# Optimization experiments

Measured on AMD Instinct MI355X. Metric: run time of the kernel, lower is better.

## Reference

```python
import jax, jax.numpy as jnp
import numpy as np

EPS = 1e-5

def _ln(x, g, b):
    mu = jnp.mean(x, axis=-1, keepdims=True)
    var = jnp.mean(jnp.square(x - mu), axis=-1, keepdims=True)
    return (x - mu) * jax.lax.rsqrt(var + EPS) * g + b

def setup_inputs() -> dict:
    B, T, D, E, H, M = 2, 2048, 1024, 8, 512, 2048
    key = jax.random.key(0)
    ks = jax.random.split(key, 24)
    s = 0.02
    inp = {}
    inp['x'] = jax.random.normal(ks[0], (B, T, D), jnp.float32)
    flat = jnp.arange(M, dtype=jnp.int32) * 2  # unique token ids over B*T
    inp['index_b'] = flat // T
    inp['index_t'] = flat % T
    # shared SwiGLU (hidden = H)
    inp['sw1'] = jax.random.normal(ks[1], (H, D), jnp.float32) * s
    inp['sb1'] = jnp.zeros((H,), jnp.float32)
    inp['sw2'] = jax.random.normal(ks[2], (H, D), jnp.float32) * s
    inp['sb2'] = jnp.zeros((H,), jnp.float32)
    inp['sw3'] = jax.random.normal(ks[3], (D, H), jnp.float32) * s
    inp['sb3'] = jnp.zeros((D,), jnp.float32)
    inp['s_ln_g'] = jnp.ones((H,), jnp.float32)
    inp['s_ln_b'] = jnp.zeros((H,), jnp.float32)
    # gates
    inp['sg_w'] = jax.random.normal(ks[4], (1, D), jnp.float32) * s
    inp['sg_b'] = jnp.zeros((1,), jnp.float32)
    inp['eg_w'] = jax.random.normal(ks[5], (E, D), jnp.float32) * s
    inp['eg_b'] = jnp.zeros((E,), jnp.float32)
    inp['exp_bias'] = jnp.zeros((E,), jnp.float32)
    # per-expert SwiGLU stacks
    inp['ew1'] = jax.random.normal(ks[6], (E, H, D), jnp.float32) * s
    inp['eb1'] = jnp.zeros((E, H), jnp.float32)
    inp['ew2'] = jax.random.normal(ks[7], (E, H, D), jnp.float32) * s
    inp['eb2'] = jnp.zeros((E, H), jnp.float32)
    inp['ew3'] = jax.random.normal(ks[8], (E, D, H), jnp.float32) * s
    inp['eb3'] = jnp.zeros((E, D), jnp.float32)
    inp['sel_ln_g'] = jnp.ones((H,), jnp.float32)
    inp['sel_ln_b'] = jnp.zeros((H,), jnp.float32)
    return inp

def _forward(x, index_b, index_t, sw1, sb1, sw2, sb2, sw3, sb3, s_ln_g, s_ln_b,
             sg_w, sg_b, eg_w, eg_b, exp_bias, ew1, eb1, ew2, eb2, ew3, eb3,
             sel_ln_g, sel_ln_b):
    # shared SwiGLU over all tokens: [B,T,D]
    x1 = jnp.einsum('btd,hd->bth', x, sw1) + sb1
    x2 = jnp.einsum('btd,hd->bth', x, sw2) + sb2
    sh = _ln(jax.nn.silu(x1) * x2, s_ln_g, s_ln_b)
    shared_out = jnp.einsum('bth,dh->btd', sh, sw3) + sb3
    # MoE tokens
    x_moe = x[index_b, index_t]  # [M,D]
    shared_scores = jax.nn.sigmoid(x_moe @ sg_w.T + sg_b)       # [M,1]
    expert_scores = jax.nn.sigmoid(x_moe @ eg_w.T + eg_b)       # [M,E]
    top1_idx = jnp.argmax(expert_scores + exp_bias, axis=-1)    # [M]
    top1_score = jnp.take_along_axis(expert_scores, top1_idx[:, None], axis=-1)  # [M,1]
    weights = jax.nn.softmax(jnp.concatenate([shared_scores, top1_score], axis=-1), axis=-1)
    shared_w, expert_w = weights[:, 0], weights[:, 1]
    shared_moe_out = shared_out[index_b, index_t] * shared_w[:, None]
    # per-expert SwiGLU computed densely for all E, then token selects its expert
    h1 = jnp.einsum('md,ehd->meh', x_moe, ew1) + eb1  # [M,E,H]
    h2 = jnp.einsum('md,ehd->meh', x_moe, ew2) + eb2
    z = _ln(jax.nn.silu(h1) * h2, sel_ln_g, sel_ln_b)
    out_all = jnp.einsum('meh,edh->med', z, ew3) + eb3  # [M,E,D]
    expert_out = jnp.take_along_axis(out_all, top1_idx[:, None, None], axis=1)[:, 0]  # [M,D]
    expert_moe_out = expert_out * expert_w[:, None]
    final_out = shared_out.at[index_b, index_t].set(shared_moe_out + expert_moe_out)
    return final_out

def reference(x, index_b, index_t, sw1, sb1, sw2, sb2, sw3, sb3, s_ln_g, s_ln_b,
              sg_w, sg_b, eg_w, eg_b, exp_bias, ew1, eb1, ew2, eb2, ew3, eb3,
              sel_ln_g, sel_ln_b):
    return _forward(x, index_b, index_t, sw1, sb1, sw2, sb2, sw3, sb3, s_ln_g, s_ln_b,
                    sg_w, sg_b, eg_w, eg_b, exp_bias, ew1, eb1, ew2, eb2, ew3, eb3,
                    sel_ln_g, sel_ln_b)
```

## Files before the change

kernel.cpp:

```cpp
#include <hip/hip_runtime.h>
#include <cstdint>

typedef unsigned short u16;
typedef __bf16 bf16x8 __attribute__((ext_vector_type(8)));
typedef float f32x4 __attribute__((ext_vector_type(4)));

#define T_SEQ  2048
#define D_DIM  1024
#define H_DIM  512
#define E_NUM  8
#define M_TOK  2048
#define BT_TOK 4096
#define MAXP   3072

static __device__ __forceinline__ u16 f2bf(float f) {
    union { float f; uint32_t u; } v; v.f = f;
    uint32_t u = v.u;
    return (u16)((u + 0x7FFFu + ((u >> 16) & 1u)) >> 16);
}
static __device__ __forceinline__ uint32_t pack2r(float a, float b) {
    union { float f; uint32_t u; } x, y; x.f = a; y.f = b;
    return ((x.u + 0x8000u) >> 16) | ((y.u + 0x8000u) & 0xffff0000u);
}

__global__ __launch_bounds__(256)
void gating_kernel(const float* __restrict__ x,
                   const int* __restrict__ ib, const int* __restrict__ itx,
                   const float* __restrict__ sgw, const float* __restrict__ sgb,
                   const float* __restrict__ egw, const float* __restrict__ egb,
                   const float* __restrict__ ebias,
                   float* __restrict__ shw, float* __restrict__ expw,
                   int* __restrict__ top1, int* __restrict__ rowidx)
{
    int m = blockIdx.x, tid = threadIdx.x;
    __shared__ float xs[D_DIM];
    __shared__ float sc[9];
    int row = ib[m] * T_SEQ + itx[m];
    if (tid == 0) rowidx[m] = row;
    const float* xr = x + (size_t)row * D_DIM;
    ((float4*)xs)[tid] = ((const float4*)xr)[tid];
    __syncthreads();
    int lane = tid & 63, w = tid >> 6;
    for (int sidx = w; sidx < 9; sidx += 4) {
        const float* wr = (sidx == 0) ? sgw : (egw + (size_t)(sidx - 1) * D_DIM);
        float acc = 0.f;
        for (int i = lane; i < D_DIM; i += 64) acc += xs[i] * wr[i];
        #pragma unroll
        for (int o = 32; o > 0; o >>= 1) acc += __shfl_xor(acc, o);
        if (lane == 0) sc[sidx] = acc;
    }
    __syncthreads();
    if (tid == 0) {
        float ss = 1.f / (1.f + expf(-(sc[0] + sgb[0])));
        float es[E_NUM];
        float best = -1e30f; int bi = 0;
        #pragma unroll
        for (int e = 0; e < E_NUM; ++e) {
            es[e] = 1.f / (1.f + expf(-(sc[1 + e] + egb[e])));
            float t = es[e] + ebias[e];
            if (t > best) { best = t; bi = e; }
        }
        float ts = es[bi];
        shw[m]  = 1.f / (1.f + expf(ts - ss));
        expw[m] = 1.f / (1.f + expf(ss - ts));
        top1[m] = bi;
    }
}

__global__ void bucket_kernel(const int* __restrict__ top1,
                              int* __restrict__ base, int* __restrict__ cnt,
                              int* __restrict__ perm)
{
    __shared__ int lc[E_NUM], lb[E_NUM + 1], cur[E_NUM];
    int tid = threadIdx.x;
    if (tid < E_NUM) { lc[tid] = 0; cur[tid] = 0; }
    __syncthreads();
    for (int m = tid; m < M_TOK; m += 256) atomicAdd(&lc[top1[m]], 1);
    __syncthreads();
    if (tid == 0) {
        int bacc = 0;
        for (int e = 0; e < E_NUM; ++e) { lb[e] = bacc; bacc += (lc[e] + 127) & ~127; }
        lb[E_NUM] = bacc;
    }
    __syncthreads();
    for (int m = tid; m < M_TOK; m += 256) {
        int e = top1[m];
        int pos = lb[e] + atomicAdd(&cur[e], 1);
        perm[pos] = m;
    }
    if (tid <= E_NUM) base[tid] = lb[tid];
    if (tid < E_NUM)  cnt[tid]  = lc[tid];
}

template<bool SEL>
__global__ __launch_bounds__(256)
void ln_kernel(const float* __restrict__ X,
               const float* __restrict__ g, const float* __restrict__ b,
               u16* __restrict__ out,
               const int* __restrict__ base, const int* __restrict__ cnt)
{
    int m = blockIdx.x;
    int tid = threadIdx.x;
    if (SEL) {
        bool valid = false;
        int tot = base[E_NUM];
        if (m < tot) {
            int e = 0;
            while (!(m >= base[e] && m < base[e + 1])) ++e;
            valid = (m - base[e]) < cnt[e];
        }
        if (!valid) {
            out[(size_t)m * H_DIM + tid] = 0;
            out[(size_t)m * H_DIM + tid + 256] = 0;
            return;
        }
    }
    const float* row = X + (size_t)m * D_DIM;
    float a0 = row[tid],       c0 = row[H_DIM + tid];
    float a1 = row[tid + 256], c1 = row[H_DIM + tid + 256];
    float v0 = (a0 / (1.f + expf(-a0))) * c0;
    float v1 = (a1 / (1.f + expf(-a1))) * c1;
    float s = v0 + v1, s2 = v0 * v0 + v1 * v1;
    #pragma unroll
    for (int o = 32; o > 0; o >>= 1) {
        s  += __shfl_xor(s, o);
        s2 += __shfl_xor(s2, o);
    }
    __shared__ float red[8];
    int w = tid >> 6;
    if ((tid & 63) == 0) { red[w] = s; red[4 + w] = s2; }
    __syncthreads();
    s  = red[0] + red[1] + red[2] + red[3];
    s2 = red[4] + red[5] + red[6] + red[7];
    float mu  = s * (1.f / H_DIM);
    float var = s2 * (1.f / H_DIM) - mu * mu;
    float inv = rsqrtf(var + 1e-5f);
    out[(size_t)m * H_DIM + tid]       = f2bf((v0 - mu) * inv * g[tid] + b[tid]);
    out[(size_t)m * H_DIM + tid + 256] = f2bf((v1 - mu) * inv * g[tid + 256] + b[tid + 256]);
}

template<int MODE, int KLEN, bool A_BF16>
__global__ __launch_bounds__(512, 2)
void gemm_kernel(const void* __restrict__ Av, int lda,
                 const float* __restrict__ W0, const float* __restrict__ W1, int nsplit,
                 const float* __restrict__ b0, const float* __restrict__ b1,
                 float* __restrict__ C,
                 const int* __restrict__ base, const int* __restrict__ cnt,
                 const int* __restrict__ perm, const int* __restrict__ rowidx,
                 const float* __restrict__ shw, const float* __restrict__ expw)
{
    constexpr int NITER = KLEN / 64;

    const int tid   = threadIdx.x;
    const int bn    = blockIdx.x;
    const int bm    = blockIdx.y;
    const int mbase = bm * 128;

    int pend = 0;
    if (MODE >= 2) {
        const int tot = base[E_NUM];
        if (mbase >= tot) return;
        int e = 0;
        while (!(mbase >= base[e] && mbase < base[e + 1])) ++e;
        pend = base[e] + cnt[e];
        if (mbase >= pend) return;
        const size_t wstride = (size_t)H_DIM * D_DIM;
        W0 += (size_t)e * wstride;
        if (MODE == 2) W1 += (size_t)e * wstride;
        b0 += e * ((MODE == 2) ? H_DIM : D_DIM);
        if (MODE == 2) b1 += e * H_DIM;
    }

    __shared__ u16 As[128 * 72];
    __shared__ u16 Bs[128 * 72];

    const int srow = tid >> 2;
    const int skq  = tid & 3;

    const float* af = nullptr; const u16* ab = nullptr;
    if (MODE == 2) {
        int p  = mbase + srow;
        int pp = (p < pend) ? p : (pend - 1);
        int grow = rowidx[perm[pp]];
        af = (const float*)Av + (size_t)grow * lda + skq * 16;
    } else if (A_BF16) {
        ab = (const u16*)Av + (size_t)(mbase + srow) * lda + skq * 16;
    } else {
        af = (const float*)Av + (size_t)(mbase + srow) * lda + skq * 16;
    }
    int n = bn * 128 + srow;
    const float* wf = ((n < nsplit) ? (W0 + (size_t)n * KLEN)
                                    : (W1 + (size_t)(n - nsplit) * KLEN)) + skq * 16;

    const int lane = tid & 63;
    const int wid  = tid >> 6;
    const int wm   = wid & 3;
    const int wn   = wid >> 2;
    const int l16  = lane & 15, quad = lane >> 4;

    f32x4 acc[2][4];
    #pragma unroll
    for (int i = 0; i < 2; ++i)
        #pragma unroll
        for (int j = 0; j < 4; ++j)
            acc[i][j] = (f32x4){0.f, 0.f, 0.f, 0.f};

    const int kstart = (bm * 5 + bn * 3) & (NITER - 1);

    float4 paf[4]; uint4 pau[2]; float4 pbf[4];
    {
        int k0 = kstart * 64;
        #pragma unroll
        for (int q = 0; q < 4; ++q) pbf[q] = *(const float4*)(wf + k0 + q * 4);
        if (A_BF16) {
            #pragma unroll
            for (int q = 0; q < 2; ++q) pau[q] = *(const uint4*)(ab + k0 + q * 8);
        } else {
            #pragma unroll
            for (int q = 0; q < 4; ++q) paf[q] = *(const float4*)(af + k0 + q * 4);
        }
    }

    for (int it = 0; it < NITER; ++it) {
        uint4 sa0, sa1, sb0, sb1;
        if (A_BF16) { sa0 = pau[0]; sa1 = pau[1]; }
        else {
            sa0.x = pack2r(paf[0].x, paf[0].y); sa0.y = pack2r(paf[0].z, paf[0].w);
            sa0.z = pack2r(paf[1].x, paf[1].y); sa0.w = pack2r(paf[1].z, paf[1].w);
            sa1.x = pack2r(paf[2].x, paf[2].y); sa1.y = pack2r(paf[2].z, paf[2].w);
            sa1.z = pack2r(paf[3].x, paf[3].y); sa1.w = pack2r(paf[3].z, paf[3].w);
        }
        sb0.x = pack2r(pbf[0].x, pbf[0].y); sb0.y = pack2r(pbf[0].z, pbf[0].w);
        sb0.z = pack2r(pbf[1].x, pbf[1].y); sb0.w = pack2r(pbf[1].z, pbf[1].w);
        sb1.x = pack2r(pbf[2].x, pbf[2].y); sb1.y = pack2r(pbf[2].z, pbf[2].w);
        sb1.z = pack2r(pbf[3].x, pbf[3].y); sb1.w = pack2r(pbf[3].z, pbf[3].w);
        *(uint4*)(As + srow * 72 + skq * 16)     = sa0;
        *(uint4*)(As + srow * 72 + skq * 16 + 8) = sa1;
        *(uint4*)(Bs + srow * 72 + skq * 16)     = sb0;
        *(uint4*)(Bs + srow * 72 + skq * 16 + 8) = sb1;
        __syncthreads();
        if (it + 1 < NITER) {
            int k0 = (((it + 1 + kstart) & (NITER - 1))) * 64;
            #pragma unroll
            for (int q = 0; q < 4; ++q) pbf[q] = *(const float4*)(wf + k0 + q * 4);
            if (A_BF16) {
                #pragma unroll
                for (int q = 0; q < 2; ++q) pau[q] = *(const uint4*)(ab + k0 + q * 8);
            } else {
                #pragma unroll
                for (int q = 0; q < 4; ++q) paf[q] = *(const float4*)(af + k0 + q * 4);
            }
        }
        #pragma unroll
        for (int kk = 0; kk < 64; kk += 32) {
            bf16x8 av[2], bv[4];
            #pragma unroll
            for (int i = 0; i < 2; ++i)
                av[i] = *(const bf16x8*)(As + (wm * 32 + i * 16 + l16) * 72 + kk + quad * 8);
            #pragma unroll
            for (int j = 0; j < 4; ++j)
                bv[j] = *(const bf16x8*)(Bs + (wn * 64 + j * 16 + l16) * 72 + kk + quad * 8);
            #pragma unroll
            for (int i = 0; i < 2; ++i)
                #pragma unroll
                for (int j = 0; j < 4; ++j)
                    acc[i][j] = __builtin_amdgcn_mfma_f32_16x16x32_bf16(av[i], bv[j], acc[i][j], 0, 0, 0);
        }
        __syncthreads();
    }

    if (MODE == 3) {
        #pragma unroll
        for (int i = 0; i < 2; ++i) {
            #pragma unroll
            for (int rr = 0; rr < 4; ++rr) {
                int p = mbase + wm * 32 + i * 16 + quad * 4 + rr;
                if (p < pend) {
                    int tok = perm[p];
                    int row = rowidx[tok];
                    float sw = shw[tok], ew = expw[tok];
                    float* outr = C + (size_t)row * D_DIM;
                    #pragma unroll
                    for (int j = 0; j < 4; ++j) {
                        int gn = bn * 128 + wn * 64 + j * 16 + l16;
                        outr[gn] = outr[gn] * sw + (acc[i][j][rr] + b0[gn]) * ew;
                    }
                }
            }
        }
    } else {
        #pragma unroll
        for (int i = 0; i < 2; ++i) {
            #pragma unroll
            for (int rr = 0; rr < 4; ++rr) {
                int gm = mbase + wm * 32 + i * 16 + quad * 4 + rr;
                float* outr = C + (size_t)gm * D_DIM;
                #pragma unroll
                for (int j = 0; j < 4; ++j) {
                    int gn = bn * 128 + wn * 64 + j * 16 + l16;
                    float bias = (gn < nsplit) ? b0[gn] : b1[gn - nsplit];
                    outr[gn] = acc[i][j][rr] + bias;
                }
            }
        }
    }
}

extern "C" void kernel_launch(void* const* d_in, const int* in_sizes, int n_in,
                              void* d_out, int out_size, void* d_ws, size_t ws_size,
                              hipStream_t stream) {
    const float* x        = (const float*)d_in[0];
    const int*   index_b  = (const int*)d_in[1];
    const int*   index_t  = (const int*)d_in[2];
    const float* sw1      = (const float*)d_in[3];
    const float* sb1      = (const float*)d_in[4];
    const float* sw2      = (const float*)d_in[5];
    const float* sb2      = (const float*)d_in[6];
    const float* sw3      = (const float*)d_in[7];
    const float* sb3      = (const float*)d_in[8];
    const float* s_ln_g   = (const float*)d_in[9];
    const float* s_ln_b   = (const float*)d_in[10];
    const float* sg_w     = (const float*)d_in[11];
    const float* sg_b     = (const float*)d_in[12];
    const float* eg_w     = (const float*)d_in[13];
    const float* eg_b     = (const float*)d_in[14];
    const float* exp_bias = (const float*)d_in[15];
    const float* ew1      = (const float*)d_in[16];
    const float* eb1      = (const float*)d_in[17];
    const float* ew2      = (const float*)d_in[18];
    const float* eb2      = (const float*)d_in[19];
    const float* ew3      = (const float*)d_in[20];
    const float* eb3      = (const float*)d_in[21];
    const float* sel_ln_g = (const float*)d_in[22];
    const float* sel_ln_b = (const float*)d_in[23];
    float* out = (float*)d_out;
    char*  ws  = (char*)d_ws;

    float* x12  = (float*)(ws + 0);
    float* h12  = x12;
    u16*   sh   = (u16*)(ws + 16777216);
    u16*   z    = sh;
    float* shw    = (float*)(ws + 20971520);
    float* expw   = shw + M_TOK;
    int*   top1   = (int*)(expw + M_TOK);
    int*   rowidx = top1 + M_TOK;
    int*   perm   = rowidx + M_TOK;
    int*   basep  = perm + MAXP;
    int*   cntp   = basep + 16;

    const int NSPLIT_NONE = 1 << 28;

    gating_kernel<<<dim3(M_TOK), dim3(256), 0, stream>>>(x, index_b, index_t,
        sg_w, sg_b, eg_w, eg_b, exp_bias, shw, expw, top1, rowidx);
    bucket_kernel<<<dim3(1), dim3(256), 0, stream>>>(top1, basep, cntp, perm);

    gemm_kernel<0, 1024, false><<<dim3(8, 32), dim3(512), 0, stream>>>(
        x, D_DIM, sw1, sw2, H_DIM, sb1, sb2, x12,
        basep, cntp, perm, rowidx, shw, expw);
    ln_kernel<false><<<dim3(BT_TOK), dim3(256), 0, stream>>>(
        x12, s_ln_g, s_ln_b, sh, basep, cntp);
    gemm_kernel<1, 512, true><<<dim3(8, 32), dim3(512), 0, stream>>>(
        sh, H_DIM, sw3, sw3, NSPLIT_NONE, sb3, sb3, out,
        basep, cntp, perm, rowidx, shw, expw);
    gemm_kernel<2, 1024, false><<<dim3(8, MAXP / 128), dim3(512), 0, stream>>>(
        x, D_DIM, ew1, ew2, H_DIM, eb1, eb2, h12,
        basep, cntp, perm, rowidx, shw, expw);
    ln_kernel<true><<<dim3(MAXP), dim3(256), 0, stream>>>(
        h12, sel_ln_g, sel_ln_b, z, basep, cntp);
    gemm_kernel<3, 512, true><<<dim3(8, MAXP / 128), dim3(512), 0, stream>>>(
        z, H_DIM, ew3, ew3, NSPLIT_NONE, eb3, eb3, out,
        basep, cntp, perm, rowidx, shw, expw);
}
```

Baseline: 279.0 us.

## Merge shared and expert up-projection GEMMs and LayerNorms into single launches

Combines the shared and expert up-projection GEMMs into one grid, and likewise the two LayerNorm passes into one kernel. To make that possible, x12/h12 and sh/z now get separate workspace buffers instead of aliasing. The global-load layout changes to 16 threads per row with float4 loads, which gives more coalesced accesses, and the rotated k-start is dropped. Launch bounds move from 2 to 4 waves per EU to raise occupancy, with a risk of register spilling.

```diff
diff --git a/kernel.cpp b/kernel.cpp
--- a/kernel.cpp
+++ b/kernel.cpp
@@ -92,32 +92,37 @@
     if (tid < E_NUM)  cnt[tid]  = lc[tid];
 }
 
-template<bool SEL>
 __global__ __launch_bounds__(256)
-void ln_kernel(const float* __restrict__ X,
-               const float* __restrict__ g, const float* __restrict__ b,
-               u16* __restrict__ out,
-               const int* __restrict__ base, const int* __restrict__ cnt)
+void ln_all_kernel(const float* __restrict__ x12, const float* __restrict__ h12,
+                   const float* __restrict__ gs, const float* __restrict__ bs,
+                   const float* __restrict__ ge, const float* __restrict__ be,
+                   u16* __restrict__ sh, u16* __restrict__ z,
+                   const int* __restrict__ base, const int* __restrict__ cnt)
 {
     int m = blockIdx.x;
     int tid = threadIdx.x;
-    if (SEL) {
+    const float* X; const float* g; const float* b; u16* out; int row;
+    if (m < BT_TOK) {
+        X = x12; g = gs; b = bs; out = sh; row = m;
+    } else {
+        row = m - BT_TOK;
+        int tot = base[E_NUM];
         bool valid = false;
-        int tot = base[E_NUM];
-        if (m < tot) {
+        if (row < tot) {
             int e = 0;
-            while (!(m >= base[e] && m < base[e + 1])) ++e;
-            valid = (m - base[e]) < cnt[e];
+            while (!(row >= base[e] && row < base[e + 1])) ++e;
+            valid = (row - base[e]) < cnt[e];
         }
         if (!valid) {
-            out[(size_t)m * H_DIM + tid] = 0;
-            out[(size_t)m * H_DIM + tid + 256] = 0;
+            z[(size_t)row * H_DIM + tid] = 0;
+            z[(size_t)row * H_DIM + tid + 256] = 0;
             return;
         }
-    }
-    const float* row = X + (size_t)m * D_DIM;
-    float a0 = row[tid],       c0 = row[H_DIM + tid];
-    float a1 = row[tid + 256], c1 = row[H_DIM + tid + 256];
+        X = h12; g = ge; b = be; out = z;
+    }
+    const float* rp = X + (size_t)row * D_DIM;
+    float a0 = rp[tid],       c0 = rp[H_DIM + tid];
+    float a1 = rp[tid + 256], c1 = rp[H_DIM + tid + 256];
     float v0 = (a0 / (1.f + expf(-a0))) * c0;
     float v1 = (a1 / (1.f + expf(-a1))) * c1;
     float s = v0 + v1, s2 = v0 * v0 + v1 * v1;
@@ -135,62 +140,185 @@
     float mu  = s * (1.f / H_DIM);
     float var = s2 * (1.f / H_DIM) - mu * mu;
     float inv = rsqrtf(var + 1e-5f);
-    out[(size_t)m * H_DIM + tid]       = f2bf((v0 - mu) * inv * g[tid] + b[tid]);
-    out[(size_t)m * H_DIM + tid + 256] = f2bf((v1 - mu) * inv * g[tid + 256] + b[tid + 256]);
-}
-
-template<int MODE, int KLEN, bool A_BF16>
-__global__ __launch_bounds__(512, 2)
-void gemm_kernel(const void* __restrict__ Av, int lda,
-                 const float* __restrict__ W0, const float* __restrict__ W1, int nsplit,
-                 const float* __restrict__ b0, const float* __restrict__ b1,
-                 float* __restrict__ C,
-                 const int* __restrict__ base, const int* __restrict__ cnt,
-                 const int* __restrict__ perm, const int* __restrict__ rowidx,
-                 const float* __restrict__ shw, const float* __restrict__ expw)
+    out[(size_t)row * H_DIM + tid]       = f2bf((v0 - mu) * inv * g[tid] + b[tid]);
+    out[(size_t)row * H_DIM + tid + 256] = f2bf((v1 - mu) * inv * g[tid + 256] + b[tid + 256]);
+}
+
+__global__ __launch_bounds__(512, 4)
+void gemm_up_kernel(const float* __restrict__ x,
+                    const float* __restrict__ sw1, const float* __restrict__ sw2,
+                    const float* __restrict__ sb1, const float* __restrict__ sb2,
+                    const float* __restrict__ ew1, const float* __restrict__ ew2,
+                    const float* __restrict__ eb1, const float* __restrict__ eb2,
+                    float* __restrict__ x12, float* __restrict__ h12,
+                    const int* __restrict__ base, const int* __restrict__ cnt,
+                    const int* __restrict__ perm, const int* __restrict__ rowidx)
 {
-    constexpr int NITER = KLEN / 64;
-
-    const int tid   = threadIdx.x;
-    const int bn    = blockIdx.x;
-    const int bm    = blockIdx.y;
+    constexpr int NITER = 1024 / 64;
+    const int tid = threadIdx.x;
+    const int bn  = blockIdx.x;
+    const int bm  = blockIdx.y;
+
+    const int sr = tid >> 4;
+    const int sc = tid & 15;
+
+    const float *W0, *W1, *B0, *B1;
+    float* Cout;
+    int mbase;
+    const float* arow[4];
+
+    if (bm < 32) {
+        mbase = bm * 128;
+        W0 = sw1; W1 = sw2; B0 = sb1; B1 = sb2;
+        Cout = x12;
+        #pragma unroll
+        for (int t = 0; t < 4; ++t)
+            arow[t] = x + (size_t)(mbase + t * 32 + sr) * D_DIM + sc * 4;
+    } else {
+        mbase = (bm - 32) * 128;
+        const int tot = base[E_NUM];
+        if (mbase >= tot) return;
+        int e = 0;
+        while (!(mbase >= base[e] && mbase < base[e + 1])) ++e;
+        const int pend = base[e] + cnt[e];
+        if (mbase >= pend) return;
+        W0 = ew1 + (size_t)e * H_DIM * D_DIM;
+        W1 = ew2 + (size_t)e * H_DIM * D_DIM;
+        B0 = eb1 + e * H_DIM;
+        B1 = eb2 + e * H_DIM;
+        Cout = h12;
+        #pragma unroll
+        for (int t = 0; t < 4; ++t) {
+            int p  = mbase + t * 32 + sr;
+            int pp = (p < pend) ? p : (pend - 1);
+            arow[t] = x + (size_t)rowidx[perm[pp]] * D_DIM + sc * 4;
+        }
+    }
+    const float* wrow[4];
+    #pragma unroll
+    for (int t = 0; t < 4; ++t) {
+        int n = bn * 128 + t * 32 + sr;
+        wrow[t] = ((n < H_DIM) ? (W0 + (size_t)n * D_DIM)
+                               : (W1 + (size_t)(n - H_DIM) * D_DIM)) + sc * 4;
+    }
+
+    __shared__ u16 As[128 * 72];
+    __shared__ u16 Bs[128 * 72];
+
+    const int lane = tid & 63;
+    const int wid  = tid >> 6;
+    const int wm   = wid & 3;
+    const int wn   = wid >> 2;
+    const int l16  = lane & 15, quad = lane >> 4;
+
+    f32x4 acc[2][4];
+    #pragma unroll
+    for (int i = 0; i < 2; ++i)
+        #pragma unroll
+        for (int j = 0; j < 4; ++j)
+            acc[i][j] = (f32x4){0.f, 0.f, 0.f, 0.f};
+
+    float4 pa[4], pb[4];
+    #pragma unroll
+    for (int t = 0; t < 4; ++t) { pa[t] = *(const float4*)(arow[t]); pb[t] = *(const float4*)(wrow[t]); }
+
+    for (int it = 0; it < NITER; ++it) {
+        #pragma unroll
+        for (int t = 0; t < 4; ++t) {
+            int r = t * 32 + sr;
+            uint2 av = { pack2r(pa[t].x, pa[t].y), pack2r(pa[t].z, pa[t].w) };
+            uint2 bv = { pack2r(pb[t].x, pb[t].y), pack2r(pb[t].z, pb[t].w) };
+            *(uint2*)(As + r * 72 + sc * 4) = av;
+            *(uint2*)(Bs + r * 72 + sc * 4) = bv;
+        }
+        __syncthreads();
+        if (it + 1 < NITER) {
+            int k0 = (it + 1) * 64;
+            #pragma unroll
+            for (int t = 0; t < 4; ++t) {
+                pa[t] = *(const float4*)(arow[t] + k0);
+                pb[t] = *(const float4*)(wrow[t] + k0);
+            }
+        }
+        #pragma unroll
+        for (int kk = 0; kk < 64; kk += 32) {
+            bf16x8 av[2], bv[4];
+            #pragma unroll
+            for (int i = 0; i < 2; ++i)
+                av[i] = *(const bf16x8*)(As + (wm * 32 + i * 16 + l16) * 72 + kk + quad * 8);
+            #pragma unroll
+            for (int j = 0; j < 4; ++j)
+                bv[j] = *(const bf16x8*)(Bs + (wn * 64 + j * 16 + l16) * 72 + kk + quad * 8);
+            #pragma unroll
+            for (int i = 0; i < 2; ++i)
+                #pragma unroll
+                for (int j = 0; j < 4; ++j)
+                    acc[i][j] = __builtin_amdgcn_mfma_f32_16x16x32_bf16(av[i], bv[j], acc[i][j], 0, 0, 0);
+        }
+        __syncthreads();
+    }
+
+    #pragma unroll
+    for (int i = 0; i < 2; ++i) {
+        #pragma unroll
+        for (int rr = 0; rr < 4; ++rr) {
+            int gm = mbase + wm * 32 + i * 16 + quad * 4 + rr;
+            float* outr = Cout + (size_t)gm * D_DIM;
+            #pragma unroll
+            for (int j = 0; j < 4; ++j) {
+                int gn = bn * 128 + wn * 64 + j * 16 + l16;
+                float bias = (gn < H_DIM) ? B0[gn] : B1[gn - H_DIM];
+                outr[gn] = acc[i][j][rr] + bias;
+            }
+        }
+    }
+}
+
+template<bool BLEND>
+__global__ __launch_bounds__(512, 4)
+void gemm_down_kernel(const u16* __restrict__ A,
+                      const float* __restrict__ W, const float* __restrict__ bb,
+                      float* __restrict__ C,
+                      const int* __restrict__ base, const int* __restrict__ cnt,
+                      const int* __restrict__ perm, const int* __restrict__ rowidx,
+                      const float* __restrict__ shw, const float* __restrict__ expw)
+{
+    constexpr int NITER = 512 / 64;
+    const int tid = threadIdx.x;
+    const int bn  = blockIdx.x;
+    const int bm  = blockIdx.y;
     const int mbase = bm * 128;
 
     int pend = 0;
-    if (MODE >= 2) {
+    if (BLEND) {
         const int tot = base[E_NUM];
         if (mbase >= tot) return;
         int e = 0;
         while (!(mbase >= base[e] && mbase < base[e + 1])) ++e;
         pend = base[e] + cnt[e];
         if (mbase >= pend) return;
-        const size_t wstride = (size_t)H_DIM * D_DIM;
-        W0 += (size_t)e * wstride;
-        if (MODE == 2) W1 += (size_t)e * wstride;
-        b0 += e * ((MODE == 2) ? H_DIM : D_DIM);
-        if (MODE == 2) b1 += e * H_DIM;
+        W  += (size_t)e * D_DIM * H_DIM;
+        bb += e * D_DIM;
+    }
+
+    const int ar = tid >> 3;
+    const int ac = tid & 7;
+    const u16* arow[2];
+    #pragma unroll
+    for (int t = 0; t < 2; ++t)
+        arow[t] = A + (size_t)(mbase + t * 64 + ar) * H_DIM + ac * 8;
+
+    const int sr = tid >> 4;
+    const int sc = tid & 15;
+    const float* wrow[4];
+    #pragma unroll
+    for (int t = 0; t < 4; ++t) {
+        int n = bn * 128 + t * 32 + sr;
+        wrow[t] = W + (size_t)n * H_DIM + sc * 4;
     }
 
     __shared__ u16 As[128 * 72];
     __shared__ u16 Bs[128 * 72];
-
-    const int srow = tid >> 2;
-    const int skq  = tid & 3;
-
-    const float* af = nullptr; const u16* ab = nullptr;
-    if (MODE == 2) {
-        int p  = mbase + srow;
-        int pp = (p < pend) ? p : (pend - 1);
-        int grow = rowidx[perm[pp]];
-        af = (const float*)Av + (size_t)grow * lda + skq * 16;
-    } else if (A_BF16) {
-        ab = (const u16*)Av + (size_t)(mbase + srow) * lda + skq * 16;
-    } else {
-        af = (const float*)Av + (size_t)(mbase + srow) * lda + skq * 16;
-    }
-    int n = bn * 128 + srow;
-    const float* wf = ((n < nsplit) ? (W0 + (size_t)n * KLEN)
-                                    : (W1 + (size_t)(n - nsplit) * KLEN)) + skq * 16;
 
     const int lane = tid & 63;
     const int wid  = tid >> 6;
@@ -205,51 +333,28 @@
         for (int j = 0; j < 4; ++j)
             acc[i][j] = (f32x4){0.f, 0.f, 0.f, 0.f};
 
-    const int kstart = (bm * 5 + bn * 3) & (NITER - 1);
-
-    float4 paf[4]; uint4 pau[2]; float4 pbf[4];
-    {
-        int k0 = kstart * 64;
-        #pragma unroll
-        for (int q = 0; q < 4; ++q) pbf[q] = *(const float4*)(wf + k0 + q * 4);
-        if (A_BF16) {
-            #pragma unroll
-            for (int q = 0; q < 2; ++q) pau[q] = *(const uint4*)(ab + k0 + q * 8);
-        } else {
-            #pragma unroll
-            for (int q = 0; q < 4; ++q) paf[q] = *(const float4*)(af + k0 + q * 4);
-        }
-    }
+    uint4 pa[2]; float4 pb[4];
+    #pragma unroll
+    for (int t = 0; t < 2; ++t) pa[t] = *(const uint4*)(arow[t]);
+    #pragma unroll
+    for (int t = 0; t < 4; ++t) pb[t] = *(const float4*)(wrow[t]);
 
     for (int it = 0; it < NITER; ++it) {
-        uint4 sa0, sa1, sb0, sb1;
-        if (A_BF16) { sa0 = pau[0]; sa1 = pau[1]; }
-        else {
-            sa0.x = pack2r(paf[0].x, paf[0].y); sa0.y = pack2r(paf[0].z, paf[0].w);
-            sa0.z = pack2r(paf[1].x, paf[1].y); sa0.w = pack2r(paf[1].z, paf[1].w);
-            sa1.x = pack2r(paf[2].x, paf[2].y); sa1.y = pack2r(paf[2].z, paf[2].w);
-            sa1.z = pack2r(paf[3].x, paf[3].y); sa1.w = pack2r(paf[3].z, paf[3].w);
-        }
-        sb0.x = pack2r(pbf[0].x, pbf[0].y); sb0.y = pack2r(pbf[0].z, pbf[0].w);
-        sb0.z = pack2r(pbf[1].x, pbf[1].y); sb0.w = pack2r(pbf[1].z, pbf[1].w);
-        sb1.x = pack2r(pbf[2].x, pbf[2].y); sb1.y = pack2r(pbf[2].z, pbf[2].w);
-        sb1.z = pack2r(pbf[3].x, pbf[3].y); sb1.w = pack2r(pbf[3].z, pbf[3].w);
-        *(uint4*)(As + srow * 72 + skq * 16)     = sa0;
-        *(uint4*)(As + srow * 72 + skq * 16 + 8) = sa1;
-        *(uint4*)(Bs + srow * 72 + skq * 16)     = sb0;
-        *(uint4*)(Bs + srow * 72 + skq * 16 + 8) = sb1;
+        #pragma unroll
+        for (int t = 0; t < 2; ++t)
+            *(uint4*)(As + (t * 64 + ar) * 72 + ac * 8) = pa[t];
+        #pragma unroll
+        for (int t = 0; t < 4; ++t) {
+            uint2 bv = { pack2r(pb[t].x, pb[t].y), pack2r(pb[t].z, pb[t].w) };
+            *(uint2*)(Bs + (t * 32 + sr) * 72 + sc * 4) = bv;
+        }
         __syncthreads();
         if (it + 1 < NITER) {
-            int k0 = (((it + 1 + kstart) & (NITER - 1))) * 64;
-            #pragma unroll
-            for (int q = 0; q < 4; ++q) pbf[q] = *(const float4*)(wf + k0 + q * 4);
-            if (A_BF16) {
-                #pragma unroll
-                for (int q = 0; q < 2; ++q) pau[q] = *(const uint4*)(ab + k0 + q * 8);
-            } else {
-                #pragma unroll
-                for (int q = 0; q < 4; ++q) paf[q] = *(const float4*)(af + k0 + q * 4);
-            }
+            int k0 = (it + 1) * 64;
+            #pragma unroll
+            for (int t = 0; t < 2; ++t) pa[t] = *(const uint4*)(arow[t] + k0);
+            #pragma unroll
+            for (int t = 0; t < 4; ++t) pb[t] = *(const float4*)(wrow[t] + k0);
         }
         #pragma unroll
         for (int kk = 0; kk < 64; kk += 32) {
@@ -269,7 +374,7 @@
         __syncthreads();
     }
 
-    if (MODE == 3) {
+    if (BLEND) {
         #pragma unroll
         for (int i = 0; i < 2; ++i) {
             #pragma unroll
@@ -283,7 +388,7 @@
                     #pragma unroll
                     for (int j = 0; j < 4; ++j) {
                         int gn = bn * 128 + wn * 64 + j * 16 + l16;
-                        outr[gn] = outr[gn] * sw + (acc[i][j][rr] + b0[gn]) * ew;
+                        outr[gn] = outr[gn] * sw + (acc[i][j][rr] + bb[gn]) * ew;
                     }
                 }
             }
@@ -298,8 +403,7 @@
                 #pragma unroll
                 for (int j = 0; j < 4; ++j) {
                     int gn = bn * 128 + wn * 64 + j * 16 + l16;
-                    float bias = (gn < nsplit) ? b0[gn] : b1[gn - nsplit];
-                    outr[gn] = acc[i][j][rr] + bias;
+                    outr[gn] = acc[i][j][rr] + bb[gn];
                 }
             }
         }
@@ -337,10 +441,10 @@
     char*  ws  = (char*)d_ws;
 
     float* x12  = (float*)(ws + 0);
-    float* h12  = x12;
-    u16*   sh   = (u16*)(ws + 16777216);
-    u16*   z    = sh;
-    float* shw    = (float*)(ws + 20971520);
+    float* h12  = (float*)(ws + 16777216);
+    u16*   sh   = (u16*)(ws + 29360128);
+    u16*   z    = (u16*)(ws + 33554432);
+    float* shw    = (float*)(ws + 36700160);
     float* expw   = shw + M_TOK;
     int*   top1   = (int*)(expw + M_TOK);
     int*   rowidx = top1 + M_TOK;
@@ -348,26 +452,20 @@
     int*   basep  = perm + MAXP;
     int*   cntp   = basep + 16;
 
-    const int NSPLIT_NONE = 1 << 28;
-
     gating_kernel<<<dim3(M_TOK), dim3(256), 0, stream>>>(x, index_b, index_t,
         sg_w, sg_b, eg_w, eg_b, exp_bias, shw, expw, top1, rowidx);
     bucket_kernel<<<dim3(1), dim3(256), 0, stream>>>(top1, basep, cntp, perm);
 
-    gemm_kernel<0, 1024, false><<<dim3(8, 32), dim3(512), 0, stream>>>(
-        x, D_DIM, sw1, sw2, H_DIM, sb1, sb2, x12,
-        basep, cntp, perm, rowidx, shw, expw);
-    ln_kernel<false><<<dim3(BT_TOK), dim3(256), 0, stream>>>(
-        x12, s_ln_g, s_ln_b, sh, basep, cntp);
-    gemm_kernel<1, 512, true><<<dim3(8, 32), dim3(512), 0, stream>>>(
-        sh, H_DIM, sw3, sw3, NSPLIT_NONE, sb3, sb3, out,
-        basep, cntp, perm, rowidx, shw, expw);
-    gemm_kernel<2, 1024, false><<<dim3(8, MAXP / 128), dim3(512), 0, stream>>>(
-        x, D_DIM, ew1, ew2, H_DIM, eb1, eb2, h12,
-        basep, cntp, perm, rowidx, shw, expw);
-    ln_kernel<true><<<dim3(MAXP), dim3(256), 0, stream>>>(
-        h12, sel_ln_g, sel_ln_b, z, basep, cntp);
-    gemm_kernel<3, 512, true><<<dim3(8, MAXP / 128), dim3(512), 0, stream>>>(
-        z, H_DIM, ew3, ew3, NSPLIT_NONE, eb3, eb3, out,
-        basep, cntp, perm, rowidx, shw, expw);
-}
+    gemm_up_kernel<<<dim3(8, 32 + MAXP / 128), dim3(512), 0, stream>>>(
+        x, sw1, sw2, sb1, sb2, ew1, ew2, eb1, eb2, x12, h12,
+        basep, cntp, perm, rowidx);
+
+    ln_all_kernel<<<dim3(BT_TOK + MAXP), dim3(256), 0, stream>>>(
+        x12, h12, s_ln_g, s_ln_b, sel_ln_g, sel_ln_b, sh, z, basep, cntp);
+
+    gemm_down_kernel<false><<<dim3(8, 32), dim3(512), 0, stream>>>(
+        sh, sw3, sb3, out, basep, cntp, perm, rowidx, shw, expw);
+
+    gemm_down_kernel<true><<<dim3(8, MAXP / 128), dim3(512), 0, stream>>>(
+        z, ew3, eb3, out, basep, cntp, perm, rowidx, shw, expw);
+}
```

Measured after the change: 266.5 us. 1.05x faster.
